# Performance work log

Measured on AMD Instinct MI355X. Metric: run time of the kernel, lower is better.

Reference implementation:

```python
import jax, jax.numpy as jnp
import numpy as np

N = 1024        # batch of tokens (module is per-token; we vmap via batched einsums)
IN = 1024       # in_features
H = 16          # num_heads
D = 64          # head_dim
BD = 512        # binary_dim
M = 8192        # num memories
OUT = H * D     # out_features
TEMP = 0.01
EPS = 1e-5


def setup_inputs() -> dict:
    key = jax.random.key(0)
    ks = jax.random.split(key, 8)
    return {
        "x": jax.random.normal(ks[0], (N, IN), jnp.float32),
        "Wq": jax.random.normal(ks[1], (OUT, IN), jnp.float32) / np.sqrt(IN).astype(np.float32),
        "bq_bias": jax.random.normal(ks[2], (OUT,), jnp.float32) * 0.01,
        "bin_proj": jax.random.normal(ks[3], (H, BD, D), jnp.float32),
        "bin_inv": jax.random.normal(ks[4], (H, D, BD), jnp.float32) / np.float32(BD),
        # binary memory codes in {-1, +1}
        "weight_matrix": jnp.sign(jax.random.normal(ks[5], (H, M, BD), jnp.float32)),
        "ln_w": jnp.ones((OUT,), jnp.float32),
        "ln_b": jnp.zeros((OUT,), jnp.float32),
    }


def reference(x, Wq, bq_bias, bin_proj, bin_inv, weight_matrix, ln_w, ln_b):
    # query projection: [N, OUT] -> [N, H, D], L2-normalize per head
    q = (x @ Wq.T + bq_bias).reshape(N, H, D)
    q = q / jnp.linalg.norm(q, axis=-1, keepdims=True)
    # sign-encode into binary space: [N, H, BD]
    code = jnp.sign(jnp.einsum('nhd,hbd->nhb', q, bin_proj))
    # cosine-transformed Hamming-similarity scores: [N, H, M]
    sim = jnp.einsum('nhb,hmb->nhm', code, weight_matrix) / np.float32(BD)
    scores = jnp.cos((np.float32(np.pi) / 2) * (1.0 - sim))
    attn = jax.nn.softmax(scores / np.float32(TEMP), axis=-1)
    # readout from binary memories, project back to real space
    out = jnp.einsum('nhm,hmb->nhb', attn, weight_matrix)
    out = jnp.einsum('nhb,hdb->nhd', out, bin_inv)
    out = out / jnp.linalg.norm(out, axis=-1, keepdims=True)
    out = out.reshape(N, OUT)
    # LayerNorm over out_features
    mu = jnp.mean(out, axis=-1, keepdims=True)
    var = jnp.var(out, axis=-1, keepdims=True)
    return (out - mu) / jnp.sqrt(var + np.float32(EPS)) * ln_w + ln_b
```

## Files before the change

kernel.cpp:

```cpp
#include <hip/hip_runtime.h>
#include <hip/hip_fp16.h>

#define NTOK 1024
#define INF  1024
#define NH   16
#define DH   64
#define BDIM 512
#define NMEM 8192
#define OUTF 1024
#define NWRD 16

typedef _Float16 f16x8 __attribute__((ext_vector_type(8)));
typedef float    f32x4 __attribute__((ext_vector_type(4)));
typedef int      i32x4 __attribute__((ext_vector_type(4)));

#define GLOAD16(G, L) __builtin_amdgcn_global_load_lds( \
    (const __attribute__((address_space(1))) unsigned int*)(G), \
    (__attribute__((address_space(3))) unsigned int*)(L), 16, 0, 0)

__device__ inline float score2(float s) {
  return 144.2695040889f * __sinf(s * 0.0030679615757712823f);
}

__global__ __launch_bounds__(256) void k_qgemm(const float* __restrict__ x,
    const float* __restrict__ Wq, const float* __restrict__ bq, float* __restrict__ q) {
  __shared__ float As[64][17];
  __shared__ float Bs[64][17];
  const int tx = threadIdx.x & 15, ty = threadIdx.x >> 4;
  const int n0 = blockIdx.y * 64, o0 = blockIdx.x * 64;
  const int r = threadIdx.x >> 2, c4 = (threadIdx.x & 3) * 4;
  float acc[4][4] = {};
  for (int k0 = 0; k0 < INF; k0 += 16) {
    float4 av = *(const float4*)&x[(size_t)(n0 + r) * INF + k0 + c4];
    float4 bv = *(const float4*)&Wq[(size_t)(o0 + r) * INF + k0 + c4];
    __syncthreads();
    As[r][c4+0] = av.x; As[r][c4+1] = av.y; As[r][c4+2] = av.z; As[r][c4+3] = av.w;
    Bs[r][c4+0] = bv.x; Bs[r][c4+1] = bv.y; Bs[r][c4+2] = bv.z; Bs[r][c4+3] = bv.w;
    __syncthreads();
    #pragma unroll
    for (int kk = 0; kk < 16; ++kk) {
      float a[4], b[4];
      #pragma unroll
      for (int i = 0; i < 4; ++i) a[i] = As[ty*4+i][kk];
      #pragma unroll
      for (int j = 0; j < 4; ++j) b[j] = Bs[tx*4+j][kk];
      #pragma unroll
      for (int i = 0; i < 4; ++i)
        #pragma unroll
        for (int j = 0; j < 4; ++j) acc[i][j] += a[i] * b[j];
    }
  }
  #pragma unroll
  for (int i = 0; i < 4; ++i) {
    const int row = n0 + ty*4 + i;
    #pragma unroll
    for (int j = 0; j < 4; ++j) {
      const int col = o0 + tx*4 + j;
      q[(size_t)row * OUTF + col] = acc[i][j] + bq[col];
    }
  }
}

__global__ __launch_bounds__(256) void k_code(const float* __restrict__ q,
    const float* __restrict__ bp, signed char* __restrict__ code_i8) {
  const int h = blockIdx.y, n0 = blockIdx.x * 16;
  __shared__ float ql[16][68];
  const int t = threadIdx.x;
  {
    const int r = t >> 4, c = (t & 15) * 4;
    float4 v = *(const float4*)&q[(size_t)(n0 + r) * OUTF + h * 64 + c];
    ql[r][c] = v.x; ql[r][c+1] = v.y; ql[r][c+2] = v.z; ql[r][c+3] = v.w;
  }
  __syncthreads();
  #pragma unroll
  for (int bb = 0; bb < 512; bb += 256) {
    const int b = bb + t;
    float bpv[64];
    const float4* src = (const float4*)&bp[((size_t)h * BDIM + b) * 64];
    #pragma unroll
    for (int j = 0; j < 16; ++j) {
      float4 v = src[j];
      bpv[j*4] = v.x; bpv[j*4+1] = v.y; bpv[j*4+2] = v.z; bpv[j*4+3] = v.w;
    }
    for (int n = 0; n < 16; ++n) {
      float dot = 0.f;
      #pragma unroll
      for (int d = 0; d < 64; ++d) dot += bpv[d] * ql[n][d];
      code_i8[((size_t)h * NTOK + n0 + n) * BDIM + b] = dot > 0.f ? 1 : -1;
    }
  }
}

__global__ __launch_bounds__(256) void k_packw(const float* __restrict__ w,
    unsigned* __restrict__ wp, signed char* __restrict__ w_i8) {
  const int row  = blockIdx.x * 4 + (threadIdx.x >> 6);
  const int lane = threadIdx.x & 63;
  const float* src = w + (size_t)row * BDIM;
  unsigned my = 0;
  #pragma unroll
  for (int kk = 0; kk < 8; ++kk) {
    float v = src[kk * 64 + lane];
    const int c = kk * 4 + (lane >> 4);
    const int p = (c & ~7) | ((c & 7) ^ (row & 7));
    w_i8[(size_t)row * BDIM + p * 16 + (lane & 15)] = v > 0.f ? 1 : -1;
    unsigned long long m = __ballot(v > 0.f);
    if ((lane >> 1) == kk) my = (lane & 1) ? (unsigned)(m >> 32) : (unsigned)m;
  }
  if (lane < 16) wp[(size_t)row * NWRD + lane] = my;
}

__global__ __launch_bounds__(256) void k_binT(const float* __restrict__ binv,
                                              float* __restrict__ bT) {
  const int h = blockIdx.y, b0 = blockIdx.x * 64;
  __shared__ float tl[64][65];
  const int t = threadIdx.x;
  #pragma unroll
  for (int i = 0; i < 4; ++i) {
    int fi = t + 256 * i;
    int d = fi >> 4, b = (fi & 15) * 4;
    float4 v = *(const float4*)&binv[((size_t)h * DH + d) * BDIM + b0 + b];
    tl[d][b] = v.x; tl[d][b+1] = v.y; tl[d][b+2] = v.z; tl[d][b+3] = v.w;
  }
  __syncthreads();
  #pragma unroll
  for (int i = 0; i < 4; ++i) {
    int fo = t + 256 * i;
    int bb = fo >> 4, dd = (fo & 15) * 4;
    float4 v = { tl[dd][bb], tl[dd+1][bb], tl[dd+2][bb], tl[dd+3][bb] };
    *(float4*)&bT[((size_t)h * BDIM + b0 + bb) * DH + dd] = v;
  }
}

__global__ __launch_bounds__(256) void k_wt(const unsigned* __restrict__ wp,
    unsigned short* __restrict__ wt, int h0) {
  const int hg = blockIdx.z, h = h0 + hg;
  const int b0 = blockIdx.y * 64, m0 = blockIdx.x * 256;
  __shared__ unsigned bits[256][2];
  const int t = threadIdx.x;
  const unsigned* src = wp + (size_t)(h * NMEM + m0 + t) * NWRD + (b0 >> 5);
  bits[t][0] = src[0]; bits[t][1] = src[1];
  __syncthreads();
  const int b = t >> 2, ms = (t & 3) * 64;
  const int wd = b >> 5, sh = b & 31;
  const int bx7 = b & 7;
  unsigned short* dst = wt + ((size_t)hg * BDIM + b0 + b) * NMEM + m0 + ms;
  #pragma unroll
  for (int g = 0; g < 8; ++g) {
    const int pg = g ^ bx7;
    const int j = ms + g * 8;
    ushort4 v0, v1;
    v0.x = ((bits[j+0][wd] >> sh) & 1) ? 0x3C00 : 0xBC00;
    v0.y = ((bits[j+1][wd] >> sh) & 1) ? 0x3C00 : 0xBC00;
    v0.z = ((bits[j+2][wd] >> sh) & 1) ? 0x3C00 : 0xBC00;
    v0.w = ((bits[j+3][wd] >> sh) & 1) ? 0x3C00 : 0xBC00;
    v1.x = ((bits[j+4][wd] >> sh) & 1) ? 0x3C00 : 0xBC00;
    v1.y = ((bits[j+5][wd] >> sh) & 1) ? 0x3C00 : 0xBC00;
    v1.z = ((bits[j+6][wd] >> sh) & 1) ? 0x3C00 : 0xBC00;
    v1.w = ((bits[j+7][wd] >> sh) & 1) ? 0x3C00 : 0xBC00;
    *(ushort4*)&dst[pg * 8]     = v0;
    *(ushort4*)&dst[pg * 8 + 4] = v1;
  }
}

__global__ __launch_bounds__(512, 2) void k_sim(const signed char* __restrict__ code_i8,
    const signed char* __restrict__ w_i8, short* __restrict__ simb,
    int h0, int gmask, int gshift) {
  const int bid = (int)blockIdx.x;
  const int hg = bid & gmask, h = h0 + hg;
  const int n0 = (bid >> gshift) * 64;
  const int t = threadIdx.x, lane = t & 63, wid = t >> 6;
  __shared__ __align__(16) signed char Bls[64 * 512];
  __shared__ float sct[513];
  __shared__ int smaxl[64];
  if (t < 64) smaxl[t] = -(1 << 30);
  for (int p = t; p < 513; p += 512)
    sct[p] = score2(2.f * (float)p - 512.f);
  const int rg = wid >> 2, mg = wid & 3;
  i32x4 afrag[2][8];
  #pragma unroll
  for (int fi = 0; fi < 2; ++fi)
    #pragma unroll
    for (int kk = 0; kk < 8; ++kk)
      afrag[fi][kk] = *(const i32x4*)(code_i8 +
          ((size_t)h * NTOK + n0 + rg * 32 + fi * 16 + (lane & 15)) * BDIM +
          kk * 64 + (lane >> 4) * 16);
  const signed char* wb = w_i8 + (size_t)h * NMEM * BDIM + (size_t)t * 16;
  signed char* const d0 = &Bls[wid * 1024];
  int vmax[2][4];
  #pragma unroll
  for (int fi = 0; fi < 2; ++fi)
    #pragma unroll
    for (int j = 0; j < 4; ++j) vmax[fi][j] = -(1 << 30);
  short* srow = simb + ((size_t)hg * NTOK + n0) * NMEM;
  for (int tile = 0; tile < 128; ++tile) {
    const signed char* s = wb + (size_t)tile * 64 * BDIM;
    __syncthreads();
    GLOAD16(s, d0); GLOAD16(s + 8192, d0 + 8192);
    GLOAD16(s + 16384, d0 + 16384); GLOAD16(s + 24576, d0 + 24576);
    __syncthreads();
    const signed char* bls = &Bls[(mg * 16 + (lane & 15)) * 512];
    i32x4 acc0 = {}, acc1 = {};
    #pragma unroll
    for (int kk = 0; kk < 8; ++kk) {
      const int c = kk * 4 + (lane >> 4);
      const int p = (c & ~7) | ((c & 7) ^ (lane & 7));
      i32x4 b = *(const i32x4*)(bls + p * 16);
      acc0 = __builtin_amdgcn_mfma_i32_16x16x64_i8(afrag[0][kk], b, acc0, 0, 0, 0);
      acc1 = __builtin_amdgcn_mfma_i32_16x16x64_i8(afrag[1][kk], b, acc1, 0, 0, 0);
    }
    const int m0 = tile * 64 + mg * 16 + (lane & 15);
    #pragma unroll
    for (int j = 0; j < 4; ++j) {
      const int r0 = rg * 32 + (lane >> 4) * 4 + j;
      srow[(size_t)r0 * NMEM + m0]        = (short)acc0[j];
      srow[(size_t)(r0 + 16) * NMEM + m0] = (short)acc1[j];
      vmax[0][j] = max(vmax[0][j], acc0[j]);
      vmax[1][j] = max(vmax[1][j], acc1[j]);
    }
  }
  #pragma unroll
  for (int fi = 0; fi < 2; ++fi)
    #pragma unroll
    for (int j = 0; j < 4; ++j) {
      int v = vmax[fi][j];
      #pragma unroll
      for (int s = 1; s < 16; s <<= 1) v = max(v, __shfl_xor(v, s));
      if ((lane & 15) == 0)
        atomicMax(&smaxl[rg * 32 + fi * 16 + (lane >> 4) * 4 + j], v);
    }
  __syncthreads();
  unsigned short* arow = (unsigned short*)srow;
  for (int it = 0; it < 16; ++it) {
    const int gw = it * 512 + t;
    const int row = gw >> 7, win = gw & 127;
    const float sm2 = sct[(smaxl[row] + 512) >> 1];
    const short* sp = srow + (size_t)row * NMEM + win * 64;
    uint4 sv[8];
    #pragma unroll
    for (int c = 0; c < 8; ++c) sv[c] = *(const uint4*)(sp + c * 8);
    const int rx = row & 7;
    unsigned short* dp = arow + (size_t)row * NMEM + win * 64;
    #pragma unroll
    for (int c = 0; c < 8; ++c) {
      unsigned ov[4];
      #pragma unroll
      for (int k = 0; k < 4; ++k) {
        const unsigned w2 = (&sv[c].x)[k];
        const int lo = (int)(short)(w2 & 0xffffu);
        const int hi = (int)(short)(w2 >> 16);
        float p0 = exp2f(sct[(lo + 512) >> 1] - sm2);
        float p1 = exp2f(sct[(hi + 512) >> 1] - sm2);
        ov[k] = (unsigned)__half_as_ushort(__float2half(p0))
              | ((unsigned)__half_as_ushort(__float2half(p1)) << 16);
      }
      *(uint4*)(dp + (c ^ rx) * 8) = make_uint4(ov[0], ov[1], ov[2], ov[3]);
    }
  }
}

__global__ __launch_bounds__(512, 2) void k_stageF(const unsigned short* __restrict__ attn,
    const unsigned short* __restrict__ wt, float* __restrict__ o1t,
    int gmask, int gshift) {
  __shared__ __align__(16) _Float16 Al[128][64];
  __shared__ __align__(16) _Float16 Bl[128][64];
  const int wg = (int)blockIdx.x;
  const int hg = wg & gmask;
  const int rest = wg >> gshift;
  const int nt = rest & 7, bt = rest >> 3;
  const int n0 = nt * 128, b0 = bt * 128;
  const int t = threadIdx.x;
  const int lane = t & 63, wid = t >> 6;
  const int wm = wid >> 2, wn = wid & 3;
  f32x4 acc[4][2];
  #pragma unroll
  for (int i = 0; i < 4; ++i)
    #pragma unroll
    for (int j = 0; j < 2; ++j) acc[i][j] = (f32x4){0.f, 0.f, 0.f, 0.f};

  const unsigned short* ag = attn + ((size_t)hg * NTOK + n0 + 16*wid + (lane >> 3)) * NMEM + (lane & 7) * 8;
  const unsigned short* bg = wt   + ((size_t)hg * BDIM + b0 + 16*wid + (lane >> 3)) * NMEM + (lane & 7) * 8;
  _Float16* al0 = &Al[16 * wid][0];
  _Float16* bl0 = &Bl[16 * wid][0];

  for (int k0 = 0; k0 < NMEM; k0 += 64) {
    __syncthreads();
    GLOAD16(ag + k0,            al0);
    GLOAD16(ag + k0 + 8 * NMEM, al0 + 8 * 64);
    GLOAD16(bg + k0,            bl0);
    GLOAD16(bg + k0 + 8 * NMEM, bl0 + 8 * 64);
    __syncthreads();
    #pragma unroll
    for (int kk = 0; kk < 64; kk += 32) {
      const int phys = (((kk >> 3) + (lane >> 4)) ^ (lane & 7)) * 8;
      f16x8 af[4], bf[2];
      #pragma unroll
      for (int fm = 0; fm < 4; ++fm)
        af[fm] = *(const f16x8*)&Al[wm*64 + fm*16 + (lane & 15)][phys];
      #pragma unroll
      for (int fn = 0; fn < 2; ++fn)
        bf[fn] = *(const f16x8*)&Bl[wn*32 + fn*16 + (lane & 15)][phys];
      #pragma unroll
      for (int fm = 0; fm < 4; ++fm)
        #pragma unroll
        for (int fn = 0; fn < 2; ++fn)
          acc[fm][fn] = __builtin_amdgcn_mfma_f32_16x16x32_f16(af[fm], bf[fn], acc[fm][fn], 0, 0, 0);
    }
  }
  #pragma unroll
  for (int fm = 0; fm < 4; ++fm) {
    const int rowb = n0 + wm*64 + fm*16 + (lane >> 4) * 4;
    #pragma unroll
    for (int fn = 0; fn < 2; ++fn) {
      const int col = b0 + wn*32 + fn*16 + (lane & 15);
      *(f32x4*)&o1t[((size_t)hg * BDIM + col) * NTOK + rowb] = acc[fm][fn];
    }
  }
}

__global__ __launch_bounds__(256) void k_proj(const float* __restrict__ o1t,
    const float* __restrict__ bT, float* __restrict__ o2, int h0) {
  const int hg = blockIdx.y, h = h0 + hg;
  const int n0 = blockIdx.x * 64;
  __shared__ float bl[128][68];
  __shared__ float ol[128][68];
  __shared__ float outl[64][68];
  __shared__ float nrm[64];
  const int t = threadIdx.x;
  const int tx = t & 15, ty = t >> 4;
  float acc[4][4] = {};
  for (int c = 0; c < 4; ++c) {
    const int bb0 = c * 128;
    __syncthreads();
    #pragma unroll
    for (int i = 0; i < 8; ++i) {
      int fi = t + 256 * i;
      int rr = fi >> 4, cc = (fi & 15) * 4;
      *(float4*)&bl[rr][cc] = *(const float4*)&bT[((size_t)h * BDIM + bb0 + rr) * DH + cc];
      *(float4*)&ol[rr][cc] = *(const float4*)&o1t[((size_t)hg * BDIM + bb0 + rr) * NTOK + n0 + cc];
    }
    __syncthreads();
    for (int bb = 0; bb < 128; ++bb) {
      float4 bd = *(const float4*)&bl[bb][tx * 4];
      float4 on = *(const float4*)&ol[bb][ty * 4];
      float ai[4] = {on.x, on.y, on.z, on.w};
      float bj[4] = {bd.x, bd.y, bd.z, bd.w};
      #pragma unroll
      for (int i = 0; i < 4; ++i)
        #pragma unroll
        for (int j = 0; j < 4; ++j) acc[i][j] += ai[i] * bj[j];
    }
  }
  __syncthreads();
  #pragma unroll
  for (int i = 0; i < 4; ++i)
    #pragma unroll
    for (int j = 0; j < 4; ++j) outl[ty*4 + i][tx*4 + j] = acc[i][j];
  __syncthreads();
  if (t < 64) {
    float s = 0.f;
    #pragma unroll
    for (int d = 0; d < 64; ++d) { float v = outl[t][d]; s += v * v; }
    nrm[t] = 1.f / sqrtf(s);
  }
  __syncthreads();
  {
    const int n = t >> 2, dg = (t & 3) * 16;
    #pragma unroll
    for (int j = 0; j < 16; ++j)
      o2[(size_t)(n0 + n) * OUTF + h * 64 + dg + j] = outl[n][dg + j] * nrm[n];
  }
}

__global__ __launch_bounds__(256) void k_ln(const float* __restrict__ o2,
    const float* __restrict__ lnw, const float* __restrict__ lnb, float* __restrict__ out) {
  const int n = blockIdx.x, t = threadIdx.x;
  __shared__ float red[4];
  float4 v = *(const float4*)&o2[(size_t)n * OUTF + t * 4];
  float s = v.x + v.y + v.z + v.w;
  const int lane = t & 63, wid = t >> 6;
  #pragma unroll
  for (int off = 32; off; off >>= 1) s += __shfl_down(s, off);
  if (lane == 0) red[wid] = s;
  __syncthreads();
  const float mu = (red[0] + red[1] + red[2] + red[3]) * (1.f / 1024.f);
  float4 d = {v.x - mu, v.y - mu, v.z - mu, v.w - mu};
  float s2 = d.x*d.x + d.y*d.y + d.z*d.z + d.w*d.w;
  #pragma unroll
  for (int off = 32; off; off >>= 1) s2 += __shfl_down(s2, off);
  __syncthreads();
  if (lane == 0) red[wid] = s2;
  __syncthreads();
  const float var = (red[0] + red[1] + red[2] + red[3]) * (1.f / 1024.f);
  const float inv = 1.f / sqrtf(var + 1e-5f);
  float4 w = *(const float4*)&lnw[t * 4];
  float4 b = *(const float4*)&lnb[t * 4];
  float4 o = { d.x*inv*w.x + b.x, d.y*inv*w.y + b.y,
               d.z*inv*w.z + b.z, d.w*inv*w.w + b.w };
  *(float4*)&out[(size_t)n * OUTF + t * 4] = o;
}

extern "C" void kernel_launch(void* const* d_in, const int* in_sizes, int n_in,
                              void* d_out, int out_size, void* d_ws, size_t ws_size,
                              hipStream_t stream) {
  (void)in_sizes; (void)n_in; (void)out_size;
  const float* x    = (const float*)d_in[0];
  const float* Wq   = (const float*)d_in[1];
  const float* bq   = (const float*)d_in[2];
  const float* bp   = (const float*)d_in[3];
  const float* binv = (const float*)d_in[4];
  const float* wm   = (const float*)d_in[5];
  const float* lnw  = (const float*)d_in[6];
  const float* lnb  = (const float*)d_in[7];
  float* outp = (float*)d_out;

  char* ws = (char*)d_ws;
  size_t off = 0;
  auto carve = [&](size_t bytes) -> char* {
    char* p = ws + off;
    off += (bytes + 255) & ~(size_t)255;
    return p;
  };
  float*       q       = (float*)      carve((size_t)NTOK * OUTF * 4);
  signed char* code_i8 = (signed char*)carve((size_t)NH * NTOK * BDIM);
  unsigned*    wpk     = (unsigned*)   carve((size_t)NH * NMEM * NWRD * 4);
  signed char* w_i8    = (signed char*)carve((size_t)NH * NMEM * BDIM);
  float*       bT      = (float*)      carve((size_t)NH * BDIM * DH * 4);
  float*       o2      = (float*)      carve((size_t)NTOK * OUTF * 4);
  const size_t fixed = off;
  const size_t per = ((size_t)BDIM * NMEM * 2 + 256)
                   + ((size_t)NTOK * NMEM * 2 + 256)
                   + ((size_t)BDIM * NTOK * 4 + 256);
  int G = 16;
  while (G > 1 && fixed + (size_t)G * per > ws_size) G >>= 1;
  unsigned short* wt   = (unsigned short*)carve((size_t)G * BDIM * NMEM * 2);
  short*          simb = (short*)         carve((size_t)G * NTOK * NMEM * 2);
  float*          o1t  = (float*)         carve((size_t)G * BDIM * NTOK * 4);
  const int gshift = __builtin_ctz(G);

  k_qgemm<<<dim3(16, 16), 256, 0, stream>>>(x, Wq, bq, q);
  k_code <<<dim3(64, 16), 256, 0, stream>>>(q, bp, code_i8);
  k_packw<<<dim3(NH * NMEM / 4), 256, 0, stream>>>(wm, wpk, w_i8);
  k_binT <<<dim3(8, 16), 256, 0, stream>>>(binv, bT);
  for (int h0 = 0; h0 < NH; h0 += G) {
    k_wt    <<<dim3(32, 8, G), 256, 0, stream>>>(wpk, wt, h0);
    k_sim   <<<dim3(16 * G),   512, 0, stream>>>(code_i8, w_i8, simb, h0, G - 1, gshift);
    k_stageF<<<dim3(32 * G),   512, 0, stream>>>((const unsigned short*)simb, wt, o1t, G - 1, gshift);
    k_proj  <<<dim3(16, G),    256, 0, stream>>>(o1t, bT, o2, h0);
  }
  k_ln<<<dim3(NTOK), 256, 0, stream>>>(o2, lnw, lnb, outp);
}
```

Measured before the change: 783.8 us.

## Retile k_sim to 32 tokens by 128 memories per block, doubling grid

The similarity kernel now gives each block 32 query rows instead of 64 and stages 128 memory rows per LDS tile instead of 64. The grid doubles to 32*G blocks, which gives more parallelism and better CU coverage. Each block now reuses every loaded code tile across half as many rows, so total global traffic for the memory codes doubles. LDS use rises to 64KB per block, which may limit occupancy at 2 blocks per CU.

Result: faster. 758.8 us (-3.2%).

```diff
diff --git a/kernel.cpp b/kernel.cpp
--- a/kernel.cpp
+++ b/kernel.cpp
@@ -167,70 +167,63 @@
     int h0, int gmask, int gshift) {
   const int bid = (int)blockIdx.x;
   const int hg = bid & gmask, h = h0 + hg;
-  const int n0 = (bid >> gshift) * 64;
+  const int n0 = (bid >> gshift) * 32;
   const int t = threadIdx.x, lane = t & 63, wid = t >> 6;
-  __shared__ __align__(16) signed char Bls[64 * 512];
+  __shared__ __align__(16) signed char Bls[128 * 512];
   __shared__ float sct[513];
-  __shared__ int smaxl[64];
-  if (t < 64) smaxl[t] = -(1 << 30);
+  __shared__ int smaxl[32];
+  if (t < 32) smaxl[t] = -(1 << 30);
   for (int p = t; p < 513; p += 512)
     sct[p] = score2(2.f * (float)p - 512.f);
   const int rg = wid >> 2, mg = wid & 3;
-  i32x4 afrag[2][8];
-  #pragma unroll
-  for (int fi = 0; fi < 2; ++fi)
-    #pragma unroll
-    for (int kk = 0; kk < 8; ++kk)
-      afrag[fi][kk] = *(const i32x4*)(code_i8 +
-          ((size_t)h * NTOK + n0 + rg * 32 + fi * 16 + (lane & 15)) * BDIM +
-          kk * 64 + (lane >> 4) * 16);
+  i32x4 afrag[8];
+  #pragma unroll
+  for (int kk = 0; kk < 8; ++kk)
+    afrag[kk] = *(const i32x4*)(code_i8 +
+        ((size_t)h * NTOK + n0 + rg * 16 + (lane & 15)) * BDIM +
+        kk * 64 + (lane >> 4) * 16);
   const signed char* wb = w_i8 + (size_t)h * NMEM * BDIM + (size_t)t * 16;
   signed char* const d0 = &Bls[wid * 1024];
-  int vmax[2][4];
-  #pragma unroll
-  for (int fi = 0; fi < 2; ++fi)
-    #pragma unroll
-    for (int j = 0; j < 4; ++j) vmax[fi][j] = -(1 << 30);
+  int vmax[4] = {-(1 << 30), -(1 << 30), -(1 << 30), -(1 << 30)};
   short* srow = simb + ((size_t)hg * NTOK + n0) * NMEM;
-  for (int tile = 0; tile < 128; ++tile) {
-    const signed char* s = wb + (size_t)tile * 64 * BDIM;
-    __syncthreads();
-    GLOAD16(s, d0); GLOAD16(s + 8192, d0 + 8192);
-    GLOAD16(s + 16384, d0 + 16384); GLOAD16(s + 24576, d0 + 24576);
-    __syncthreads();
-    const signed char* bls = &Bls[(mg * 16 + (lane & 15)) * 512];
-    i32x4 acc0 = {}, acc1 = {};
-    #pragma unroll
-    for (int kk = 0; kk < 8; ++kk) {
-      const int c = kk * 4 + (lane >> 4);
-      const int p = (c & ~7) | ((c & 7) ^ (lane & 7));
-      i32x4 b = *(const i32x4*)(bls + p * 16);
-      acc0 = __builtin_amdgcn_mfma_i32_16x16x64_i8(afrag[0][kk], b, acc0, 0, 0, 0);
-      acc1 = __builtin_amdgcn_mfma_i32_16x16x64_i8(afrag[1][kk], b, acc1, 0, 0, 0);
-    }
-    const int m0 = tile * 64 + mg * 16 + (lane & 15);
-    #pragma unroll
-    for (int j = 0; j < 4; ++j) {
-      const int r0 = rg * 32 + (lane >> 4) * 4 + j;
-      srow[(size_t)r0 * NMEM + m0]        = (short)acc0[j];
-      srow[(size_t)(r0 + 16) * NMEM + m0] = (short)acc1[j];
-      vmax[0][j] = max(vmax[0][j], acc0[j]);
-      vmax[1][j] = max(vmax[1][j], acc1[j]);
-    }
-  }
-  #pragma unroll
-  for (int fi = 0; fi < 2; ++fi)
-    #pragma unroll
-    for (int j = 0; j < 4; ++j) {
-      int v = vmax[fi][j];
-      #pragma unroll
-      for (int s = 1; s < 16; s <<= 1) v = max(v, __shfl_xor(v, s));
-      if ((lane & 15) == 0)
-        atomicMax(&smaxl[rg * 32 + fi * 16 + (lane >> 4) * 4 + j], v);
-    }
+  for (int tile = 0; tile < 64; ++tile) {
+    const signed char* s = wb + (size_t)tile * 128 * BDIM;
+    __syncthreads();
+    #pragma unroll
+    for (int seg = 0; seg < 8; ++seg)
+      GLOAD16(s + seg * 8192, d0 + seg * 8192);
+    __syncthreads();
+    #pragma unroll
+    for (int msub = 0; msub < 2; ++msub) {
+      const signed char* bls = &Bls[(mg * 32 + msub * 16 + (lane & 15)) * 512];
+      i32x4 acc = {};
+      #pragma unroll
+      for (int kk = 0; kk < 8; ++kk) {
+        const int c = kk * 4 + (lane >> 4);
+        const int p = (c & ~7) | ((c & 7) ^ (lane & 7));
+        i32x4 b = *(const i32x4*)(bls + p * 16);
+        acc = __builtin_amdgcn_mfma_i32_16x16x64_i8(afrag[kk], b, acc, 0, 0, 0);
+      }
+      const int m0 = tile * 128 + mg * 32 + msub * 16 + (lane & 15);
+      #pragma unroll
+      for (int j = 0; j < 4; ++j) {
+        const int r0 = rg * 16 + (lane >> 4) * 4 + j;
+        srow[(size_t)r0 * NMEM + m0] = (short)acc[j];
+        vmax[j] = max(vmax[j], acc[j]);
+      }
+    }
+  }
+  #pragma unroll
+  for (int j = 0; j < 4; ++j) {
+    int v = vmax[j];
+    #pragma unroll
+    for (int s = 1; s < 16; s <<= 1) v = max(v, __shfl_xor(v, s));
+    if ((lane & 15) == 0)
+      atomicMax(&smaxl[rg * 16 + (lane >> 4) * 4 + j], v);
+  }
   __syncthreads();
   unsigned short* arow = (unsigned short*)srow;
-  for (int it = 0; it < 16; ++it) {
+  for (int it = 0; it < 8; ++it) {
     const int gw = it * 512 + t;
     const int row = gw >> 7, win = gw & 127;
     const float sm2 = sct[(smaxl[row] + 512) >> 1];
@@ -443,7 +436,7 @@
   k_binT <<<dim3(8, 16), 256, 0, stream>>>(binv, bT);
   for (int h0 = 0; h0 < NH; h0 += G) {
     k_wt    <<<dim3(32, 8, G), 256, 0, stream>>>(wpk, wt, h0);
-    k_sim   <<<dim3(16 * G),   512, 0, stream>>>(code_i8, w_i8, simb, h0, G - 1, gshift);
+    k_sim   <<<dim3(32 * G),   512, 0, stream>>>(code_i8, w_i8, simb, h0, G - 1, gshift);
     k_stageF<<<dim3(32 * G),   512, 0, stream>>>((const unsigned short*)simb, wt, o1t, G - 1, gshift);
     k_proj  <<<dim3(16, G),    256, 0, stream>>>(o1t, bT, o2, h0);
   }
```
